# Optimization experiments

Measured on AMD Instinct MI355X. Metric: run time of the kernel, lower is better.

## Reference

```python
import jax, jax.numpy as jnp
import numpy as np

K = 16  # neighborhood size


def _eigen_ratio(pts, k):
    """pts: [B, N, 3] -> ratio lambda_max / lambda_mid per point, [B, N]."""
    pts = pts[..., :3]
    # pairwise squared distances [B, N, N]
    sq = jnp.sum(pts * pts, axis=-1)  # [B, N]
    d2 = sq[:, :, None] + sq[:, None, :] - 2.0 * jnp.einsum('bnd,bmd->bnm', pts, pts)
    # k nearest neighbors (self included, as in KNN(x, x))
    _, idx = jax.lax.top_k(-d2, k)  # idx: [B, N, k] int32
    # gather neighbor coordinates: [B, N, k, 3]
    neighbors = jax.vmap(lambda p, i: p[i])(pts, idx)
    mean = jnp.mean(neighbors, axis=2, keepdims=True)
    diff = neighbors - mean  # [B, N, k, 3]
    # covariance = mean over k of outer products -> [B, N, 3, 3]
    cov = jnp.einsum('bnki,bnkj->bnij', diff, diff) / k
    ev = jnp.linalg.eigvalsh(cov)  # ascending: [..., 3]
    return ev[..., 2] / ev[..., 1]


def setup_inputs() -> dict:
    key = jax.random.key(0)
    kx, ky = jax.random.split(key)
    x = jax.random.normal(kx, (2, 8192, 3), dtype=jnp.float32)
    y = jax.random.normal(ky, (2, 8192, 3), dtype=jnp.float32)
    return {"x": x, "y": y}


def reference(x, y):
    er1 = _eigen_ratio(x, K)  # [B, N]
    er2 = _eigen_ratio(y, K)
    res = jnp.mean((er1 - er2) ** 2, axis=-1)  # mean over points
    return jnp.mean(res)  # reduction='mean' over batch
```

## Files before the change

kernel.cpp:

```cpp
#include <hip/hip_runtime.h>
#include <hip/hip_bf16.h>
#include <math.h>

#define NPTS   8192
#define KNN    16
#define G      16
#define NCELL  (G * G * G)
#define NCHUNK 128
#define NPART  4

__constant__ float c_B[17] = {
    -1e30f,
    -1.5341205f, -1.1503494f, -0.8871466f, -0.6744898f, -0.4887764f,
    -0.3186394f, -0.1573107f,  0.0f,        0.1573107f,  0.3186394f,
     0.4887764f,  0.6744898f,  0.8871466f,  1.1503494f,  1.5341205f,
     1e30f
};

__device__ __forceinline__ int cellOf(float v) {
    int c = 0;
#pragma unroll
    for (int i = 1; i <= 15; ++i) c += (v >= c_B[i]) ? 1 : 0;
    return c;
}

__device__ __forceinline__ int spread3(int v) {
    v = (v | (v << 4)) & 0x0C3;
    v = (v | (v << 2)) & 0x249;
    return v;
}

__device__ __forceinline__ int mortonCell(float px, float py, float pz) {
    return (spread3(cellOf(px)) << 2) | (spread3(cellOf(py)) << 1) | spread3(cellOf(pz));
}

__device__ __forceinline__ float dpp_prev_f(float v) {
    int r = __builtin_amdgcn_update_dpp(0, __float_as_int(v), 0x111, 0xF, 0xF, false);
    return __int_as_float(r);
}
__device__ __forceinline__ int dpp_prev_i(int v) {
    return __builtin_amdgcn_update_dpp(0, v, 0x111, 0xF, 0xF, false);
}

__device__ __forceinline__ float sum16(float v) {
    int b;
    b = __builtin_amdgcn_update_dpp(0, __float_as_int(v), 0xB1, 0xF, 0xF, false);
    v += __int_as_float(b);
    b = __builtin_amdgcn_update_dpp(0, __float_as_int(v), 0x4E, 0xF, 0xF, false);
    v += __int_as_float(b);
    b = __builtin_amdgcn_update_dpp(0, __float_as_int(v), 0x141, 0xF, 0xF, false);
    v += __int_as_float(b);
    b = __builtin_amdgcn_update_dpp(0, __float_as_int(v), 0x140, 0xF, 0xF, false);
    v += __int_as_float(b);
    return v;
}

__global__ __launch_bounds__(1024) void countscan_kernel(
    const float* __restrict__ x, const float* __restrict__ y,
    unsigned int* __restrict__ cellcnt ) {

    __shared__ unsigned int h[NCELL];
    __shared__ unsigned int scanbuf[1024];
    const int tid   = threadIdx.x;
    const int cloud = blockIdx.x;
    const float* __restrict__ src = (cloud < 2 ? x : y) + (size_t)(cloud & 1) * NPTS * 3;

    for (int i = tid; i < NCELL; i += 1024) h[i] = 0;
    __syncthreads();
#pragma unroll
    for (int k = 0; k < 8; ++k) {
        int p = (k << 10) | tid;
        atomicAdd(&h[mortonCell(src[3 * p], src[3 * p + 1], src[3 * p + 2])], 1u);
    }
    __syncthreads();

    unsigned int c0 = h[4 * tid], c1 = h[4 * tid + 1];
    unsigned int c2 = h[4 * tid + 2], c3 = h[4 * tid + 3];
    unsigned int ssum = c0 + c1 + c2 + c3;
    scanbuf[tid] = ssum;
    __syncthreads();
    for (int d = 1; d < 1024; d <<= 1) {
        unsigned int a = scanbuf[tid];
        unsigned int w = (tid >= d) ? scanbuf[tid - d] : 0;
        __syncthreads();
        scanbuf[tid] = a + w;
        __syncthreads();
    }
    unsigned int excl = scanbuf[tid] - ssum;
    unsigned int* cc = cellcnt + cloud * NCELL;
    cc[4 * tid]     = excl;
    cc[4 * tid + 1] = excl + c0;
    cc[4 * tid + 2] = excl + c0 + c1;
    cc[4 * tid + 3] = excl + c0 + c1 + c2;
}

__global__ __launch_bounds__(256) void scatter_kernel(
    const float* __restrict__ x, const float* __restrict__ y,
    unsigned int* __restrict__ cellcnt,
    float4* __restrict__ Ps, unsigned short* __restrict__ origids) {

    const int tid   = threadIdx.x;
    const int cloud = blockIdx.x >> 2;
    const int part  = blockIdx.x & 3;
    const float* __restrict__ src = (cloud < 2 ? x : y) + (size_t)(cloud & 1) * NPTS * 3;
    unsigned int* cc = cellcnt + cloud * NCELL;

#pragma unroll
    for (int k = 0; k < 8; ++k) {
        int p = (part << 11) | (k << 8) | tid;
        float px = src[3 * p], py = src[3 * p + 1], pz = src[3 * p + 2];
        int c = mortonCell(px, py, pz);
        unsigned int pos = atomicAdd(&cc[c], 1u);
        Ps[(cloud << 13) + pos] = make_float4(-2.f * px, -2.f * py, -2.f * pz,
                                              px * px + py * py + pz * pz);
        origids[(cloud << 13) + pos] = (unsigned short)p;
    }
}

__global__ __launch_bounds__(256) void aabb_kernel(
    const float4* __restrict__ Ps, float* __restrict__ aabbG ) {

    const int tid  = threadIdx.x;
    const int lane = tid & 63;
    const int w    = (blockIdx.x << 2) | (tid >> 6);
    const int cloud = w >> 7;
    const int c     = w & 127;

    float4 f = Ps[(cloud << 13) | (c << 6) | lane];
    float px = -0.5f * f.x, py = -0.5f * f.y, pz = -0.5f * f.z;
    float lx = px, hx = px, ly = py, hy = py, lz = pz, hz = pz;
#pragma unroll
    for (int s = 1; s < 64; s <<= 1) {
        lx = fminf(lx, __shfl_xor(lx, s)); hx = fmaxf(hx, __shfl_xor(hx, s));
        ly = fminf(ly, __shfl_xor(ly, s)); hy = fmaxf(hy, __shfl_xor(hy, s));
        lz = fminf(lz, __shfl_xor(lz, s)); hz = fmaxf(hz, __shfl_xor(hz, s));
    }
    if (lane == 0) {
        float* ab = aabbG + cloud * (6 * NCHUNK);
        ab[0 * NCHUNK + c] = lx; ab[1 * NCHUNK + c] = hx;
        ab[2 * NCHUNK + c] = ly; ab[3 * NCHUNK + c] = hy;
        ab[4 * NCHUNK + c] = lz; ab[5 * NCHUNK + c] = hz;
    }
}

__global__ __launch_bounds__(64) void knn_cov_kernel(
    const float4* __restrict__ Ps, const unsigned short* __restrict__ origids,
    const float* __restrict__ aabbG, float* __restrict__ cov,
    unsigned int* __restrict__ counter) {

    const int lane = threadIdx.x;
    const int wid  = blockIdx.x;
    const int cloud = wid >> 13;
    const int s     = wid & (NPTS - 1);

    if (wid == 0 && lane == 0) *counter = 0;

    const float4* __restrict__ Pc = Ps + (cloud << 13);
    const float* __restrict__ ab = aabbG + cloud * (6 * NCHUNK);
    const float4 qp = Pc[s];
    const float sqq = qp.w;
    const float qx = -0.5f * qp.x, qy = -0.5f * qp.y, qz = -0.5f * qp.z;
    const int co = s >> 6;

    float bval[2];
#pragma unroll
    for (int g = 0; g < 2; ++g) {
        int c = (g << 6) | lane;
        float dxl = fmaxf(0.f, fmaxf(ab[c] - qx, qx - ab[NCHUNK + c]));
        float dyl = fmaxf(0.f, fmaxf(ab[2 * NCHUNK + c] - qy, qy - ab[3 * NCHUNK + c]));
        float dzl = fmaxf(0.f, fmaxf(ab[4 * NCHUNK + c] - qz, qz - ab[5 * NCHUNK + c]));
        bval[g] = dxl * dxl + dyl * dyl + dzl * dzl;
    }
    unsigned long long rem0 = ~0ull, rem1 = ~0ull;
    if (co < 64) rem0 &= ~(1ull << co); else rem1 &= ~(1ull << (co - 64));

    auto dual_argmin = [&](unsigned long long l0, unsigned long long l1,
                           int& cidA, int& cidB, bool& hasB) {
        unsigned int k0 = ((l0 >> lane) & 1)
            ? ((__float_as_uint(bval[0]) & 0xFFFFFF80u) | (unsigned)lane) : 0xFFFFFFFFu;
        unsigned int k1 = ((l1 >> lane) & 1)
            ? ((__float_as_uint(bval[1]) & 0xFFFFFF80u) | (unsigned)(64 + lane)) : 0xFFFFFFFFu;
        unsigned int a = min(k0, k1), b = max(k0, k1);
#pragma unroll
        for (int w = 1; w < 64; w <<= 1) {
            unsigned int oa = __shfl_xor(a, w);
            unsigned int ob = __shfl_xor(b, w);
            unsigned int mn = min(a, oa), mx = max(a, oa);
            unsigned int c2 = (a < oa) ? b : ob;
            a = mn; b = min(mx, c2);
        }
        cidA = (int)(a & 127u);
        hasB = (b != 0xFFFFFFFFu); cidB = (int)(b & 127u);
    };
    auto clear_rem = [&](int cid) {
        if (cid < 64) rem0 &= ~(1ull << cid); else rem1 &= ~(1ull << (cid - 64));
    };
    auto bound_of = [&](int cid) {
        return __int_as_float(__builtin_amdgcn_readlane(
            __float_as_int(bval[cid >> 6]), cid & 63));
    };
    auto popPair = [&](unsigned long long& l0, unsigned long long& l1,
                       int& cA, int& cB, bool& hB) {
        if (__popcll(l0) + __popcll(l1) <= 2) {
            if (l0) { cA = __builtin_ctzll(l0); l0 &= l0 - 1; }
            else    { cA = 64 + __builtin_ctzll(l1); l1 &= l1 - 1; }
            if (l0)      { cB = __builtin_ctzll(l0); l0 &= l0 - 1; hB = true; }
            else if (l1) { cB = 64 + __builtin_ctzll(l1); l1 &= l1 - 1; hB = true; }
            else hB = false;
        } else {
            dual_argmin(l0, l1, cA, cB, hB);
            if (cA < 64) l0 &= ~(1ull << cA); else l1 &= ~(1ull << (cA - 64));
            if (hB) { if (cB < 64) l0 &= ~(1ull << cB); else l1 &= ~(1ull << (cB - 64)); }
        }
        clear_rem(cA);
        if (hB) clear_rem(cB);
    };

    unsigned long long t0 = rem0, t1 = rem1;
    int pA, pB; bool hPB;
    popPair(t0, t1, pA, pB, hPB);
    float4 pfA = Pc[(pA << 6) | lane];
    float4 pfB = Pc[(pB << 6) | lane];

    float valV, thr;
    int   idxV;
    {
        int pos = (co << 6) | lane;
        float4 f = Pc[pos];
        float k = fmaf(qx, f.x, fmaf(qy, f.y, fmaf(qz, f.z, sqq + f.w)));
        int p = pos;
#pragma unroll
        for (int size = 2; size <= 64; size <<= 1) {
#pragma unroll
            for (int stride = size >> 1; stride >= 1; stride >>= 1) {
                float ok = __shfl_xor(k, stride);
                int   op = __shfl_xor(p, stride);
                bool up = ((lane & size) == 0);
                bool lower = ((lane & stride) == 0);
                bool want_min = (up == lower);
                bool take = want_min ? (ok < k) : (ok > k);
                k = take ? ok : k;
                p = take ? op : p;
            }
        }
        valV = __shfl(k, lane & 15);
        idxV = __shfl(p, lane & 15);
        thr  = __shfl(k, 15);
    }

    auto process = [&](float4 f, int cid) {
        float d2 = fmaf(qx, f.x, fmaf(qy, f.y, fmaf(qz, f.z, sqq + f.w)));
        unsigned long long m = __ballot(d2 < thr);
        if (m) {
            do {
                int li = __builtin_ctzll(m); m &= m - 1;
                float sv = __int_as_float(
                    __builtin_amdgcn_readlane(__float_as_int(d2), li));
                int sj = (cid << 6) | li;
                float pv = dpp_prev_f(valV);
                int   pi = dpp_prev_i(idxV);
                bool keep  = (valV <= sv);
                bool fromv = ((lane & 15) == 0) || (pv <= sv);
                float nv = keep ? valV : (fromv ? sv : pv);
                int   ni = keep ? idxV : (fromv ? sj : pi);
                valV = nv; idxV = ni;
            } while (m);
            thr = __int_as_float(__builtin_amdgcn_readlane(__float_as_int(valV), 15));
        }
    };

    if (bound_of(pA) < thr) process(pfA, pA);
    if (hPB && bound_of(pB) < thr) process(pfB, pB);

    for (;;) {
        unsigned long long live0 = rem0 & __ballot(bval[0] < thr);
        unsigned long long live1 = rem1 & __ballot(bval[1] < thr);
        if (!(live0 | live1)) break;

        int cidA, cidB, cidC = 0, cidD = 0;
        bool hasB, hasC = false, hasD = false;
        popPair(live0, live1, cidA, cidB, hasB);
        if (live0 | live1) { popPair(live0, live1, cidC, cidD, hasD); hasC = true; }

        float4 fA = Pc[(cidA << 6) | lane];
        float4 fB, fC, fD;
        if (hasB) fB = Pc[(cidB << 6) | lane];
        if (hasC) fC = Pc[(cidC << 6) | lane];
        if (hasD) fD = Pc[(cidD << 6) | lane];

        process(fA, cidA);
        if (hasB && bound_of(cidB) < thr) process(fB, cidB);
        if (hasC && bound_of(cidC) < thr) process(fC, cidC);
        if (hasD && bound_of(cidD) < thr) process(fD, cidD);
    }

    float4 nf = Pc[idxV];
    float nx = -0.5f * nf.x, ny = -0.5f * nf.y, nz = -0.5f * nf.z;

    const float invk = 1.0f / KNN;
    float mx = sum16(nx) * invk;
    float my = sum16(ny) * invk;
    float mz = sum16(nz) * invk;

    float dx = nx - mx, dy = ny - my, dz = nz - mz;
    float c00 = sum16(dx * dx) * invk, c01 = sum16(dx * dy) * invk, c02 = sum16(dx * dz) * invk;
    float c11 = sum16(dy * dy) * invk, c12 = sum16(dy * dz) * invk, c22 = sum16(dz * dz) * invk;

    if (lane == 0) {
        int orig = origids[(cloud << 13) + s];
        float* cp = cov + ((size_t)(cloud << 13) + orig) * 6;
        *(float2*)(cp)     = make_float2(c00, c01);
        *(float2*)(cp + 2) = make_float2(c02, c11);
        *(float2*)(cp + 4) = make_float2(c12, c22);
    }
}

__device__ double eig_ratio(const float* __restrict__ cp) {
    double a00 = cp[0], a01 = cp[1], a02 = cp[2];
    double a11 = cp[3], a12 = cp[4], a22 = cp[5];

    double qm = (a00 + a11 + a22) * (1.0 / 3.0);
    double p1 = a01 * a01 + a02 * a02 + a12 * a12;
    double b00 = a00 - qm, b11 = a11 - qm, b22 = a22 - qm;
    double p2 = b00 * b00 + b11 * b11 + b22 * b22 + 2.0 * p1;

    if (p2 <= 0.0) return 1.0;
    double p = sqrt(p2 * (1.0 / 6.0));
    double inv = 1.0 / p;
    double m00 = b00 * inv, m11 = b11 * inv, m22 = b22 * inv;
    double m01 = a01 * inv, m02 = a02 * inv, m12 = a12 * inv;
    double detB = m00 * (m11 * m22 - m12 * m12)
                - m01 * (m01 * m22 - m12 * m02)
                + m02 * (m01 * m12 - m11 * m02);
    double r = 0.5 * detB;
    r = fmin(1.0, fmax(-1.0, r));
    double phi = acos(r) * (1.0 / 3.0);
    double e1 = qm + 2.0 * p * cos(phi);
    double e3 = qm + 2.0 * p * cos(phi + 2.0943951023931953);
    double e2 = 3.0 * qm - e1 - e3;
    return e1 / e2;
}

#define EIG_BLOCKS 64

__global__ __launch_bounds__(256) void eigred_kernel(const float* __restrict__ cov,
                                                     double* __restrict__ partial,
                                                     unsigned int* __restrict__ counter,
                                                     float* __restrict__ out) {
    __shared__ double sb[256];
    __shared__ bool islast;
    const int i = blockIdx.x * 256 + threadIdx.x;
    double r1 = eig_ratio(cov + (size_t)i * 6);
    double r2 = eig_ratio(cov + (size_t)(2 * NPTS + i) * 6);
    double d = r1 - r2;
    sb[threadIdx.x] = d * d;
    __syncthreads();
    for (int s2 = 128; s2 > 0; s2 >>= 1) {
        if (threadIdx.x < s2) sb[threadIdx.x] += sb[threadIdx.x + s2];
        __syncthreads();
    }
    if (threadIdx.x == 0) {
        partial[blockIdx.x] = sb[0];
        __threadfence();
        islast = (atomicAdd(counter, 1u) == EIG_BLOCKS - 1);
    }
    __syncthreads();
    if (islast && threadIdx.x < 64) {
        __threadfence();
        double v = ((volatile double*)partial)[threadIdx.x];
#pragma unroll
        for (int w = 1; w < 64; w <<= 1) v += __shfl_xor(v, w);
        if (threadIdx.x == 0) out[0] = (float)(v / (double)(2 * NPTS));
    }
}

extern "C" void kernel_launch(void* const* d_in, const int* in_sizes, int n_in,
                              void* d_out, int out_size, void* d_ws, size_t ws_size,
                              hipStream_t stream) {
    const float* x = (const float*)d_in[0];
    const float* y = (const float*)d_in[1];
    char* ws = (char*)d_ws;

    float4*         Ps      = (float4*)(ws);
    unsigned short* origids = (unsigned short*)(ws + 524288);
    float*          aabbG   = (float*)(ws + 589824);
    float*          cov     = (float*)(ws + 602112);
    unsigned int*   cellcnt = (unsigned int*)(ws + 1388544);
    double*         partial = (double*)(ws + 1454080);
    unsigned int*   counter = (unsigned int*)(ws + 1454592);
    float*          out     = (float*)d_out;

    countscan_kernel<<<4, 1024, 0, stream>>>(x, y, cellcnt);
    scatter_kernel<<<4 * NPART, 256, 0, stream>>>(x, y, cellcnt, Ps, origids);
    aabb_kernel<<<128, 256, 0, stream>>>(Ps, aabbG);
    knn_cov_kernel<<<4 * NPTS, 64, 0, stream>>>(Ps, origids, aabbG, cov, counter);
    eigred_kernel<<<EIG_BLOCKS, 256, 0, stream>>>(cov, partial, counter, out);
}
```

Measured before the change: 92.87 us.

## Use DPP wave-min argmin, tighten per-candidate threshold, and fetch two chunks per iteration

Replaces the shuffle-based dual argmin with two DPP-based wave minimum reductions. The insertion loop now re-checks each candidate against a threshold that is refreshed after every insert, so candidates that no longer qualify are skipped. The traversal loop fetches and processes two chunks per iteration instead of four, which re-evaluates the live set more often and prunes more chunks, at the cost of less memory-level parallelism from batched loads. The per-insert readlane of the threshold adds serial latency inside the inner loop.

```diff
diff --git a/kernel.cpp b/kernel.cpp
--- a/kernel.cpp
+++ b/kernel.cpp
@@ -55,6 +55,18 @@
     return v;
 }
 
+__device__ __forceinline__ unsigned int waveMinU32(unsigned int v) {
+    const int ID = (int)0xFFFFFFFF;
+    int t;
+    t = __builtin_amdgcn_update_dpp(ID, (int)v, 0xB1,  0xF, 0xF, false); v = min(v, (unsigned)t);
+    t = __builtin_amdgcn_update_dpp(ID, (int)v, 0x4E,  0xF, 0xF, false); v = min(v, (unsigned)t);
+    t = __builtin_amdgcn_update_dpp(ID, (int)v, 0x141, 0xF, 0xF, false); v = min(v, (unsigned)t);
+    t = __builtin_amdgcn_update_dpp(ID, (int)v, 0x140, 0xF, 0xF, false); v = min(v, (unsigned)t);
+    t = __builtin_amdgcn_update_dpp(ID, (int)v, 0x142, 0xF, 0xF, false); v = min(v, (unsigned)t);
+    t = __builtin_amdgcn_update_dpp(ID, (int)v, 0x143, 0xF, 0xF, false); v = min(v, (unsigned)t);
+    return (unsigned int)__builtin_amdgcn_readlane((int)v, 63);
+}
+
 __global__ __launch_bounds__(1024) void countscan_kernel(
     const float* __restrict__ x, const float* __restrict__ y,
     unsigned int* __restrict__ cellcnt ) {
@@ -174,22 +186,21 @@
     unsigned long long rem0 = ~0ull, rem1 = ~0ull;
     if (co < 64) rem0 &= ~(1ull << co); else rem1 &= ~(1ull << (co - 64));
 
-    auto dual_argmin = [&](unsigned long long l0, unsigned long long l1,
-                           int& cidA, int& cidB, bool& hasB) {
-        unsigned int k0 = ((l0 >> lane) & 1)
+    auto keys_of = [&](unsigned long long l0, unsigned long long l1,
+                       unsigned int& k0, unsigned int& k1) {
+        k0 = ((l0 >> lane) & 1)
             ? ((__float_as_uint(bval[0]) & 0xFFFFFF80u) | (unsigned)lane) : 0xFFFFFFFFu;
-        unsigned int k1 = ((l1 >> lane) & 1)
+        k1 = ((l1 >> lane) & 1)
             ? ((__float_as_uint(bval[1]) & 0xFFFFFF80u) | (unsigned)(64 + lane)) : 0xFFFFFFFFu;
-        unsigned int a = min(k0, k1), b = max(k0, k1);
-#pragma unroll
-        for (int w = 1; w < 64; w <<= 1) {
-            unsigned int oa = __shfl_xor(a, w);
-            unsigned int ob = __shfl_xor(b, w);
-            unsigned int mn = min(a, oa), mx = max(a, oa);
-            unsigned int c2 = (a < oa) ? b : ob;
-            a = mn; b = min(mx, c2);
-        }
+    };
+    auto argmin2 = [&](unsigned long long l0, unsigned long long l1,
+                       int& cidA, int& cidB, bool& hasB) {
+        unsigned int k0, k1;
+        keys_of(l0, l1, k0, k1);
+        unsigned int a = waveMinU32(min(k0, k1));
         cidA = (int)(a & 127u);
+        if (lane == (cidA & 63)) { if (cidA < 64) k0 = 0xFFFFFFFFu; else k1 = 0xFFFFFFFFu; }
+        unsigned int b = waveMinU32(min(k0, k1));
         hasB = (b != 0xFFFFFFFFu); cidB = (int)(b & 127u);
     };
     auto clear_rem = [&](int cid) {
@@ -208,7 +219,7 @@
             else if (l1) { cB = 64 + __builtin_ctzll(l1); l1 &= l1 - 1; hB = true; }
             else hB = false;
         } else {
-            dual_argmin(l0, l1, cA, cB, hB);
+            argmin2(l0, l1, cA, cB, hB);
             if (cA < 64) l0 &= ~(1ull << cA); else l1 &= ~(1ull << (cA - 64));
             if (hB) { if (cB < 64) l0 &= ~(1ull << cB); else l1 &= ~(1ull << (cB - 64)); }
         }
@@ -251,11 +262,11 @@
     auto process = [&](float4 f, int cid) {
         float d2 = fmaf(qx, f.x, fmaf(qy, f.y, fmaf(qz, f.z, sqq + f.w)));
         unsigned long long m = __ballot(d2 < thr);
-        if (m) {
-            do {
-                int li = __builtin_ctzll(m); m &= m - 1;
-                float sv = __int_as_float(
-                    __builtin_amdgcn_readlane(__float_as_int(d2), li));
+        while (m) {
+            int li = __builtin_ctzll(m); m &= m - 1;
+            float sv = __int_as_float(
+                __builtin_amdgcn_readlane(__float_as_int(d2), li));
+            if (sv < thr) {
                 int sj = (cid << 6) | li;
                 float pv = dpp_prev_f(valV);
                 int   pi = dpp_prev_i(idxV);
@@ -264,8 +275,8 @@
                 float nv = keep ? valV : (fromv ? sv : pv);
                 int   ni = keep ? idxV : (fromv ? sj : pi);
                 valV = nv; idxV = ni;
-            } while (m);
-            thr = __int_as_float(__builtin_amdgcn_readlane(__float_as_int(valV), 15));
+                thr = __int_as_float(__builtin_amdgcn_readlane(__float_as_int(valV), 15));
+            }
         }
     };
 
@@ -277,21 +288,15 @@
         unsigned long long live1 = rem1 & __ballot(bval[1] < thr);
         if (!(live0 | live1)) break;
 
-        int cidA, cidB, cidC = 0, cidD = 0;
-        bool hasB, hasC = false, hasD = false;
+        int cidA, cidB; bool hasB;
         popPair(live0, live1, cidA, cidB, hasB);
-        if (live0 | live1) { popPair(live0, live1, cidC, cidD, hasD); hasC = true; }
 
         float4 fA = Pc[(cidA << 6) | lane];
-        float4 fB, fC, fD;
+        float4 fB;
         if (hasB) fB = Pc[(cidB << 6) | lane];
-        if (hasC) fC = Pc[(cidC << 6) | lane];
-        if (hasD) fD = Pc[(cidD << 6) | lane];
 
         process(fA, cidA);
         if (hasB && bound_of(cidB) < thr) process(fB, cidB);
-        if (hasC && bound_of(cidC) < thr) process(fC, cidC);
-        if (hasD && bound_of(cidD) < thr) process(fD, cidD);
     }
 
     float4 nf = Pc[idxV];
```

Result: faster. 90.52 us (-2.5%).
